# Kernel optimization log

Measured on AMD Instinct MI355X. Metric: run time of the kernel, lower is better.

## Reference

```python
import jax, jax.numpy as jnp
import numpy as np

EPS = 1e-5  # BatchNorm2d default eps

def setup_inputs() -> dict:
    key = jax.random.key(0)
    k1, k2, k3, k4 = jax.random.split(key, 4)
    B, Cin, Cout, T, V = 64, 64, 128, 300, 25
    x = jax.random.normal(k1, (B, Cin, T, V), dtype=jnp.float32)
    adj = jax.random.uniform(k2, (V, V), dtype=jnp.float32)
    # Conv2d(kernel_size=1) weight (Cout, Cin), kaiming-ish scale
    W = jax.random.normal(k3, (Cout, Cin), dtype=jnp.float32) * (1.0 / np.sqrt(Cin))
    b = jnp.zeros((Cout,), dtype=jnp.float32)
    gamma = jnp.ones((Cout,), dtype=jnp.float32)
    beta = jnp.zeros((Cout,), dtype=jnp.float32)
    return {"x": x, "adj": adj, "W": W, "b": b, "gamma": gamma, "beta": beta}

def reference(x, adj, W, b, gamma, beta):
    # x: (B, C, T, V); graph aggregation over joints: matmul with adj on last dim
    xg = jnp.einsum('bctv,vw->bctw', x, adj)
    # 1x1 conv == per-(t,v) channel projection
    y = jnp.einsum('bctv,oc->botv', xg, W) + b[None, :, None, None]
    # BatchNorm2d (training mode): per-channel stats over (B, T, V), biased var
    mean = jnp.mean(y, axis=(0, 2, 3), keepdims=True)
    var = jnp.mean((y - mean) ** 2, axis=(0, 2, 3), keepdims=True)
    yn = (y - mean) * jax.lax.rsqrt(var + EPS)
    out = jax.nn.relu(gamma[None, :, None, None] * yn + beta[None, :, None, None])
    return out
```

## Files before the change

kernel.cpp:

```cpp
#include <hip/hip_runtime.h>
#include <hip/hip_bf16.h>
#include <stdint.h>

typedef __attribute__((ext_vector_type(8)))  short   short8;
typedef __attribute__((ext_vector_type(16))) float   floatx16;
typedef __attribute__((ext_vector_type(4)))  float   floatx4;

#define B_    64
#define CIN   64
#define COUT  128
#define T_    300
#define V_    25
#define NRED  (B_ * T_ * V_)
#define NSLOTS 32
#define NT    12
#define EPS   1e-5f

__device__ __forceinline__ uint32_t pk2(float a, float b) {
    union { __hip_bfloat162 h; uint32_t u; } c;
    c.h = __float22bfloat162_rn(make_float2(a, b));
    return c.u;
}

__device__ __forceinline__ floatx16 fzero16() {
    floatx16 z;
#pragma unroll
    for (int i = 0; i < 16; ++i) z[i] = 0.f;
    return z;
}

__device__ __forceinline__ int div25(int n) { return (n * 5243) >> 17; }

__device__ __forceinline__ void cvt_hb(const floatx16 h, int q, short8 hb[2]) {
    uint32_t pk[8], pp[8];
#pragma unroll
    for (int i = 0; i < 8; ++i) pk[i] = pk2(h[2 * i], h[2 * i + 1]);
#pragma unroll
    for (int i = 0; i < 8; ++i) pp[i] = (uint32_t)__shfl_xor((int)pk[i], 32, 64);
#pragma unroll
    for (int s = 0; s < 2; ++s) {
        union { short8 sv; uint32_t u[4]; } F;
        F.u[0] = q ? pp[4 * s + 2] : pk[4 * s];
        F.u[1] = q ? pp[4 * s + 3] : pk[4 * s + 1];
        F.u[2] = q ? pk[4 * s + 2] : pp[4 * s];
        F.u[3] = q ? pk[4 * s + 3] : pp[4 * s + 1];
        hb[s] = F.sv;
    }
}

__device__ __forceinline__ void build_const_frags(const float* __restrict__ W,
                                                  const float* __restrict__ adj,
                                                  int wave, int ln, int q,
                                                  short8 wf[4], short8 af[2]) {
    const float* wr = W + (32 * wave + ln) * CIN;
#pragma unroll
    for (int kk = 0; kk < 4; ++kk) {
        int c0 = 16 * kk + 8 * q;
        floatx4 a = *(const floatx4*)(wr + c0);
        floatx4 b = *(const floatx4*)(wr + c0 + 4);
        union { short8 sv; uint32_t u[4]; } F;
        F.u[0] = pk2(a[0], a[1]); F.u[1] = pk2(a[2], a[3]);
        F.u[2] = pk2(b[0], b[1]); F.u[3] = pk2(b[2], b[3]);
        wf[kk] = F.sv;
    }
#pragma unroll
    for (int s = 0; s < 2; ++s) {
        union { short8 sv; uint32_t u[4]; } F;
#pragma unroll
        for (int p = 0; p < 4; ++p) {
            int v0 = 16 * s + 8 * q + 2 * p;
            float e0 = (v0     < V_ && ln < V_) ? adj[v0 * V_ + ln]       : 0.f;
            float e1 = (v0 + 1 < V_ && ln < V_) ? adj[(v0 + 1) * V_ + ln] : 0.f;
            F.u[p] = pk2(e0, e1);
        }
        af[s] = F.sv;
    }
}

__device__ __forceinline__ void stage_x(const float* __restrict__ xb, int t4,
                                        float* __restrict__ ldsx, int tid) {
#pragma unroll
    for (int i = 0; i < 7; ++i) {
        int cid = i * 256 + tid;
        if (i < 6 || tid < 64) {
            int c  = div25(cid);
            int ch = cid - 25 * c;
            *(floatx4*)&ldsx[c * 100 + 4 * ch] =
                *(const floatx4*)(xb + c * 7500 + t4 * 25 + 4 * ch);
        }
    }
}

__device__ __forceinline__ void build_xa_lds(const float* __restrict__ ldsx,
                                             int tloc, int vcl, int q, short8 xa[4]) {
    const float* base = ldsx + tloc * 25 + vcl;
#pragma unroll
    for (int kk = 0; kk < 4; ++kk) {
        union { short8 sv; uint32_t u[4]; } F;
#pragma unroll
        for (int p = 0; p < 4; ++p) {
            int c0 = 16 * kk + 8 * q + 2 * p;
            F.u[p] = pk2(base[c0 * 100], base[(c0 + 1) * 100]);
        }
        xa[kk] = F.sv;
    }
}

__device__ __forceinline__ floatx16 compute_yt(const short8 xa[4], const short8 wf[4],
                                               const short8 af[2], int q) {
    floatx16 h = fzero16();
#pragma unroll
    for (int kk = 0; kk < 4; ++kk)
        h = __builtin_amdgcn_mfma_f32_32x32x16_bf16(xa[kk], wf[kk], h, 0, 0, 0);
    short8 hb[2];
    cvt_hb(h, q, hb);
    floatx16 y = fzero16();
#pragma unroll
    for (int s = 0; s < 2; ++s)
        y = __builtin_amdgcn_mfma_f32_32x32x16_bf16(af[s], hb[s], y, 0, 0, 0);
    return y;
}

__global__ __launch_bounds__(256, 3) void pass1_kernel(
    const float* __restrict__ x, const float* __restrict__ adj,
    const float* __restrict__ W,
    float* __restrict__ psum, float* __restrict__ psq)
{
    __shared__ __attribute__((aligned(16))) float ldsx[6400];

    const int tid  = threadIdx.x;
    const int wave = tid >> 6;
    const int lane = tid & 63;
    const int q    = lane >> 5;
    const int ln   = lane & 31;
    const int b    = blockIdx.y;
    const int tbase = blockIdx.x * NT;

    short8 wf[4], af[2];
    build_const_frags(W, adj, wave, ln, q, wf, af);
    const int vcl = ln < V_ ? ln : V_ - 1;
    const float* xb = x + (size_t)b * (CIN * T_ * V_);

    float sum = 0.f, sq = 0.f;
    for (int g = 0; g < NT / 4; ++g) {
        const int t4 = tbase + 4 * g;
        stage_x(xb, t4, ldsx, tid);
        __syncthreads();
#pragma unroll
        for (int tloc = 0; tloc < 4; ++tloc) {
            short8 xa[4];
            build_xa_lds(ldsx, tloc, vcl, q, xa);
            floatx16 y = compute_yt(xa, wf, af, q);
#pragma unroll
            for (int r = 0; r < 16; ++r) { sum += y[r]; sq += y[r] * y[r]; }
        }
        __syncthreads();
    }

    sum += __shfl_xor(sum, 32, 64);
    sq  += __shfl_xor(sq,  32, 64);
    if (q == 0) {
        int slot = (blockIdx.y * 25 + blockIdx.x) & (NSLOTS - 1);
        atomicAdd(&psum[slot * COUT + 32 * wave + ln], sum);
        atomicAdd(&psq [slot * COUT + 32 * wave + ln], sq);
    }
}

__global__ __launch_bounds__(256, 3) void pass2_kernel(
    const float* __restrict__ x, const float* __restrict__ adj,
    const float* __restrict__ W,
    const float* __restrict__ gamma, const float* __restrict__ beta,
    const float* __restrict__ psum, const float* __restrict__ psq,
    float* __restrict__ out)
{
    __shared__ __attribute__((aligned(16))) float ldsx[6400];

    const int tid  = threadIdx.x;
    const int wave = tid >> 6;
    const int lane = tid & 63;
    const int q    = lane >> 5;
    const int ln   = lane & 31;
    const int b    = blockIdx.y;
    const int tbase = blockIdx.x * NT;
    const int o_l  = 32 * wave + ln;

    short8 wf[4], af[2];
    build_const_frags(W, adj, wave, ln, q, wf, af);

    float s0 = 0.f, ss = 0.f;
#pragma unroll 4
    for (int k = 0; k < NSLOTS; ++k) {
        s0 += psum[k * COUT + o_l];
        ss += psq [k * COUT + o_l];
    }
    const float mean = s0 / (float)NRED;
    const float var  = ss / (float)NRED - mean * mean;
    const float inv  = rsqrtf(var + EPS);
    const float sc0  = gamma[o_l] * inv;
    const float sh0  = beta[o_l] - mean * sc0;

    float scr[16], shr[16];
#pragma unroll
    for (int r = 0; r < 16; ++r) {
        int src = (r & 3) + 8 * (r >> 2) + 4 * q;
        scr[r] = __shfl(sc0, src, 64);
        shr[r] = __shfl(sh0, src, 64);
    }

    const int vcl = ln < V_ ? ln : V_ - 1;
    const float* xb = x + (size_t)b * (CIN * T_ * V_);
    float* const ob = out + (size_t)(b * COUT + 32 * wave + 4 * q) * (T_ * V_) + ln;

    for (int g = 0; g < NT / 4; ++g) {
        const int t4 = tbase + 4 * g;
        stage_x(xb, t4, ldsx, tid);
        __syncthreads();
#pragma unroll
        for (int tloc = 0; tloc < 4; ++tloc) {
            short8 xa[4];
            build_xa_lds(ldsx, tloc, vcl, q, xa);
            floatx16 h = fzero16();
#pragma unroll
            for (int kk = 0; kk < 4; ++kk)
                h = __builtin_amdgcn_mfma_f32_32x32x16_bf16(xa[kk], wf[kk], h, 0, 0, 0);
            short8 hb[2];
            cvt_hb(h, q, hb);
            floatx16 y = fzero16();
#pragma unroll
            for (int s2 = 0; s2 < 2; ++s2)
                y = __builtin_amdgcn_mfma_f32_32x32x16_bf16(hb[s2], af[s2], y, 0, 0, 0);
            if (ln < V_) {
                float* pt = ob + (size_t)(t4 + tloc) * V_;
#pragma unroll
                for (int r = 0; r < 16; ++r) {
                    const int orow = (r & 3) + 8 * (r >> 2);
                    float v = scr[r] * y[r] + shr[r];
                    pt[(size_t)orow * (T_ * V_)] = v > 0.f ? v : 0.f;
                }
            }
        }
        __syncthreads();
    }
}


extern "C" void kernel_launch(void* const* d_in, const int* in_sizes, int n_in,
                              void* d_out, int out_size, void* d_ws, size_t ws_size,
                              hipStream_t stream) {
    const float* x     = (const float*)d_in[0];
    const float* adj   = (const float*)d_in[1];
    const float* W     = (const float*)d_in[2];
    const float* gamma = (const float*)d_in[4];
    const float* beta  = (const float*)d_in[5];
    float* out = (float*)d_out;

    float* psum = (float*)d_ws;
    float* psq  = (float*)((char*)d_ws + NSLOTS * COUT * sizeof(float));

    hipMemsetAsync(psum, 0, 2 * NSLOTS * COUT * sizeof(float), stream);

    dim3 grid(T_ / NT, B_);
    pass1_kernel<<<grid, 256, 0, stream>>>(x, adj, W, psum, psq);
    pass2_kernel<<<grid, 256, 0, stream>>>(x, adj, W, gamma, beta, psum, psq, out);
}
```

Before: 472.1 us.

## Stage x in LDS as transposed packed bf16 pairs with XOR swizzle

The x tile is now converted to bf16 pairs while staging and stored transposed per (t,v) row, with an XOR swizzle on channel groups. Each MFMA A-fragment can then be read with a single 128-bit LDS load instead of eight strided scalar loads plus packing. This halves the LDS footprint and moves the conversion work into the staging step. The cost is more scattered 32-bit LDS stores during staging, which may hit bank conflicts.

```diff
diff --git a/kernel.cpp b/kernel.cpp
--- a/kernel.cpp
+++ b/kernel.cpp
@@ -2,9 +2,10 @@
 #include <hip/hip_bf16.h>
 #include <stdint.h>
 
-typedef __attribute__((ext_vector_type(8)))  short   short8;
-typedef __attribute__((ext_vector_type(16))) float   floatx16;
-typedef __attribute__((ext_vector_type(4)))  float   floatx4;
+typedef __attribute__((ext_vector_type(8)))  short    short8;
+typedef __attribute__((ext_vector_type(16))) float    floatx16;
+typedef __attribute__((ext_vector_type(4)))  float    floatx4;
+typedef __attribute__((ext_vector_type(4)))  uint32_t uint4v;
 
 #define B_    64
 #define CIN   64
@@ -29,8 +30,6 @@
     return z;
 }
 
-__device__ __forceinline__ int div25(int n) { return (n * 5243) >> 17; }
-
 __device__ __forceinline__ void cvt_hb(const floatx16 h, int q, short8 hb[2]) {
     uint32_t pk[8], pp[8];
 #pragma unroll
@@ -77,31 +76,37 @@
     }
 }
 
-__device__ __forceinline__ void stage_x(const float* __restrict__ xb, int t4,
-                                        float* __restrict__ ldsx, int tid) {
-#pragma unroll
-    for (int i = 0; i < 7; ++i) {
+__device__ __forceinline__ void stage_xT(const float* __restrict__ xb, int t4,
+                                         uint32_t* __restrict__ lds, int tid) {
+#pragma unroll
+    for (int i = 0; i < 4; ++i) {
         int cid = i * 256 + tid;
-        if (i < 6 || tid < 64) {
-            int c  = div25(cid);
-            int ch = cid - 25 * c;
-            *(floatx4*)&ldsx[c * 100 + 4 * ch] =
-                *(const floatx4*)(xb + c * 7500 + t4 * 25 + 4 * ch);
-        }
-    }
-}
-
-__device__ __forceinline__ void build_xa_lds(const float* __restrict__ ldsx,
-                                             int tloc, int vcl, int q, short8 xa[4]) {
-    const float* base = ldsx + tloc * 25 + vcl;
+        if (i < 3 || tid < 32) {
+            int ch = cid >> 5;
+            int cp = cid & 31;
+            const float* p0 = xb + (2 * cp) * 7500 + t4 * 25 + 4 * ch;
+            floatx4 a = *(const floatx4*)p0;
+            floatx4 b = *(const floatx4*)(p0 + 7500);
+            const int g  = cp >> 2;
+            const int c2 = cp & 3;
+#pragma unroll
+            for (int k = 0; k < 4; ++k) {
+                int tv = 4 * ch + k;
+                lds[tv * 32 + (((g ^ (tv & 7)) << 2) | c2)] = pk2(a[k], b[k]);
+            }
+        }
+    }
+}
+
+__device__ __forceinline__ void build_xa_ldsT(const uint32_t* __restrict__ lds,
+                                              int tloc, int vcl, int q, short8 xa[4]) {
+    const int tv = tloc * 25 + vcl;
+    const uint32_t* row = lds + tv * 32;
+    const int x7 = tv & 7;
 #pragma unroll
     for (int kk = 0; kk < 4; ++kk) {
-        union { short8 sv; uint32_t u[4]; } F;
-#pragma unroll
-        for (int p = 0; p < 4; ++p) {
-            int c0 = 16 * kk + 8 * q + 2 * p;
-            F.u[p] = pk2(base[c0 * 100], base[(c0 + 1) * 100]);
-        }
+        union { short8 sv; uint4v u4; } F;
+        F.u4 = *(const uint4v*)(row + (((q + 2 * kk) ^ x7) << 2));
         xa[kk] = F.sv;
     }
 }
@@ -126,7 +131,7 @@
     const float* __restrict__ W,
     float* __restrict__ psum, float* __restrict__ psq)
 {
-    __shared__ __attribute__((aligned(16))) float ldsx[6400];
+    __shared__ __attribute__((aligned(16))) uint32_t ldsx2[3200];
 
     const int tid  = threadIdx.x;
     const int wave = tid >> 6;
@@ -144,12 +149,12 @@
     float sum = 0.f, sq = 0.f;
     for (int g = 0; g < NT / 4; ++g) {
         const int t4 = tbase + 4 * g;
-        stage_x(xb, t4, ldsx, tid);
+        stage_xT(xb, t4, ldsx2, tid);
         __syncthreads();
 #pragma unroll
         for (int tloc = 0; tloc < 4; ++tloc) {
             short8 xa[4];
-            build_xa_lds(ldsx, tloc, vcl, q, xa);
+            build_xa_ldsT(ldsx2, tloc, vcl, q, xa);
             floatx16 y = compute_yt(xa, wf, af, q);
 #pragma unroll
             for (int r = 0; r < 16; ++r) { sum += y[r]; sq += y[r] * y[r]; }
@@ -173,7 +178,7 @@
     const float* __restrict__ psum, const float* __restrict__ psq,
     float* __restrict__ out)
 {
-    __shared__ __attribute__((aligned(16))) float ldsx[6400];
+    __shared__ __attribute__((aligned(16))) uint32_t ldsx2[3200];
 
     const int tid  = threadIdx.x;
     const int wave = tid >> 6;
@@ -213,12 +218,12 @@
 
     for (int g = 0; g < NT / 4; ++g) {
         const int t4 = tbase + 4 * g;
-        stage_x(xb, t4, ldsx, tid);
+        stage_xT(xb, t4, ldsx2, tid);
         __syncthreads();
 #pragma unroll
         for (int tloc = 0; tloc < 4; ++tloc) {
             short8 xa[4];
-            build_xa_lds(ldsx, tloc, vcl, q, xa);
+            build_xa_ldsT(ldsx2, tloc, vcl, q, xa);
             floatx16 h = fzero16();
 #pragma unroll
             for (int kk = 0; kk < 4; ++kk)
```

New measurement: 466.2 us. Within noise of the previous version (-1.3%).
